# Kernel tuning notes

Hardware: AMD Instinct MI355X
Metric: run time of the kernel (lower is better)

## Reference

```python
import jax, jax.numpy as jnp
import numpy as np

DIM = 1024
HEADS = 16
DIM_HEAD = 64
INNER = HEADS * DIM_HEAD  # 1024
EPS = 1e-5


def layer_norm(x, g, b):
    mu = jnp.mean(x, axis=-1, keepdims=True)
    var = jnp.var(x, axis=-1, keepdims=True)
    return (x - mu) * jax.lax.rsqrt(var + EPS) * g + b


def setup_inputs() -> dict:
    key = jax.random.key(0)
    ks = jax.random.split(key, 8)
    s = 0.02
    return {
        "x": jax.random.normal(ks[0], (2, 2048, DIM), dtype=jnp.float32),
        "w_qkv": jax.random.normal(ks[1], (DIM, 3 * INNER), dtype=jnp.float32) * s,
        "w_out": jax.random.normal(ks[2], (INNER, DIM), dtype=jnp.float32) * s,
        "b_out": jnp.zeros((DIM,), jnp.float32),
        "g1": jnp.ones((DIM,), jnp.float32),
        "bt1": jnp.zeros((DIM,), jnp.float32),
        "g2": jnp.ones((DIM,), jnp.float32),
        "bt2": jnp.zeros((DIM,), jnp.float32),
        "w1": jax.random.normal(ks[3], (DIM, DIM), dtype=jnp.float32) * s,  # ff hidden = dim_out = DIM
        "b1": jnp.zeros((DIM,), jnp.float32),
        "w2": jax.random.normal(ks[4], (DIM, DIM), dtype=jnp.float32) * s,
        "b2": jnp.zeros((DIM,), jnp.float32),
    }


def reference(x, w_qkv, w_out, b_out, g1, bt1, g2, bt2, w1, b1, w2, b2):
    b, n, _ = x.shape
    scale = DIM_HEAD ** (-0.5)
    x_in = x
    xl = layer_norm(x, g1, bt1)
    qkv = xl @ w_qkv  # [b, n, 3*inner]
    q, k, v = jnp.split(qkv, 3, axis=-1)
    def split_heads(t):
        return t.reshape(b, n, HEADS, DIM_HEAD).transpose(0, 2, 1, 3)  # b h n d
    q, k, v = map(split_heads, (q, k, v))
    dots = jnp.einsum('bhid,bhjd->bhij', q, k) * scale
    attn = jax.nn.softmax(dots, axis=-1)
    out = jnp.einsum('bhij,bhjd->bhid', attn, v)
    out = out.transpose(0, 2, 1, 3).reshape(b, n, INNER)
    out = out @ w_out + b_out
    out = out + x_in
    h = layer_norm(out, g2, bt2)
    h = jax.nn.gelu(h @ w1 + b1, approximate=False) @ w2 + b2
    return h + out
```

## Files before the change

kernel.cpp:

```cpp
#include <hip/hip_runtime.h>
#include <math.h>

typedef __attribute__((ext_vector_type(4))) float f32x4;
typedef __attribute__((ext_vector_type(8))) short bf16x8;
typedef __attribute__((ext_vector_type(8))) unsigned short u16x8;

#define DIM 1024
#define SEQ 2048
#define NHEADS 16
#define DH 64

__device__ __forceinline__ unsigned short f2bf(float f) {
    unsigned int u = __builtin_bit_cast(unsigned int, f);
    u += 0x7fffu + ((u >> 16) & 1u);
    return (unsigned short)(u >> 16);
}

__device__ __forceinline__ float bf2f(unsigned short s) {
    unsigned int u = (unsigned int)s << 16;
    return __builtin_bit_cast(float, u);
}

__device__ __forceinline__ unsigned int cvt_pk_bf16(float lo, float hi) {
    unsigned int r;
    asm("v_cvt_pk_bf16_f32 %0, %1, %2" : "=v"(r) : "v"(lo), "v"(hi));
    return r;
}

__device__ __forceinline__ float fexp2(float x) {
    float r;
    asm("v_exp_f32 %0, %1" : "=v"(r) : "v"(x));
    return r;
}

__device__ __forceinline__ void gld16(const unsigned short* g, unsigned short* l) {
    __builtin_amdgcn_global_load_lds((const __attribute__((address_space(1))) void*)g,
                                     (__attribute__((address_space(3))) void*)l, 16, 0, 0);
}

__global__ __launch_bounds__(256) void wtrans_all(const float* __restrict__ wq,
                                                  const float* __restrict__ wo,
                                                  const float* __restrict__ wf1,
                                                  const float* __restrict__ wf2,
                                                  unsigned short* __restrict__ oq,
                                                  unsigned short* __restrict__ oo,
                                                  unsigned short* __restrict__ of1,
                                                  unsigned short* __restrict__ of2, float sc) {
    int z = blockIdx.z;
    int bxi = blockIdx.x;
    if (z > 0 && bxi >= 32) return;
    const float* w = z == 0 ? wq : z == 1 ? wo : z == 2 ? wf1 : wf2;
    unsigned short* wt = z == 0 ? oq : z == 1 ? oo : z == 2 ? of1 : of2;
    int N = z == 0 ? 3072 : 1024;
    int scale_n = z == 0 ? 1024 : 0;
    const int K = 1024;
    __shared__ float t[32][33];
    int tid = threadIdx.x;
    int n0 = bxi * 32, k0 = blockIdx.y * 32;
    int c = tid & 31, rb = tid >> 5;
#pragma unroll
    for (int i = 0; i < 4; ++i) {
        int r = rb + i * 8;
        t[r][c] = w[(size_t)(k0 + r) * N + n0 + c];
    }
    __syncthreads();
#pragma unroll
    for (int i = 0; i < 4; ++i) {
        int r = rb + i * 8;
        float v = t[c][r];
        if (n0 + r < scale_n) v *= sc;
        wt[(size_t)(n0 + r) * K + k0 + c] = f2bf(v);
    }
}

__global__ __launch_bounds__(256) void ln_kernel(const float* __restrict__ x,
                                                 const float* __restrict__ g,
                                                 const float* __restrict__ bt,
                                                 unsigned short* __restrict__ o) {
    int row = blockIdx.x, tid = threadIdx.x;
    const float4* xr = (const float4*)(x + (size_t)row * DIM);
    float4 v = xr[tid];
    float s1 = v.x + v.y + v.z + v.w;
    float s2 = v.x * v.x + v.y * v.y + v.z * v.z + v.w * v.w;
#pragma unroll
    for (int m = 32; m >= 1; m >>= 1) {
        s1 += __shfl_xor(s1, m);
        s2 += __shfl_xor(s2, m);
    }
    __shared__ float r1[4], r2[4];
    int w = tid >> 6;
    if ((tid & 63) == 0) { r1[w] = s1; r2[w] = s2; }
    __syncthreads();
    s1 = r1[0] + r1[1] + r1[2] + r1[3];
    s2 = r2[0] + r2[1] + r2[2] + r2[3];
    float mu = s1 * (1.0f / DIM);
    float var = s2 * (1.0f / DIM) - mu * mu;
    float rstd = rsqrtf(var + 1e-5f);
    float4 g4 = ((const float4*)g)[tid];
    float4 b4 = ((const float4*)bt)[tid];
    ushort4 ov;
    ov.x = f2bf((v.x - mu) * rstd * g4.x + b4.x);
    ov.y = f2bf((v.y - mu) * rstd * g4.y + b4.y);
    ov.z = f2bf((v.z - mu) * rstd * g4.z + b4.z);
    ov.w = f2bf((v.w - mu) * rstd * g4.w + b4.w);
    *(ushort4*)(o + (size_t)row * DIM + tid * 4) = ov;
}

template <int BN, int BK, int OBF, int BIAS, int GELU_, int RESID>
__global__ __launch_bounds__(256) void gemm_kernel(const unsigned short* __restrict__ A,
                                                   const unsigned short* __restrict__ BT,
                                                   void* __restrict__ C,
                                                   const float* __restrict__ bias,
                                                   const float* __restrict__ resid,
                                                   int M, int N, int K, int nbx) {
    constexpr int U = BK / 8;
    constexpr int NAU = 128 * U;
    constexpr int NBU = BN * U;
    constexpr int PT = (NAU + NBU) / 256;
    constexpr int NJ = BN / 32;
    constexpr int KK = BK / 32;
    __shared__ unsigned short As[3][128 * BK];
    __shared__ unsigned short Bs[3][BN * BK];
    int tid = threadIdx.x;
    int lane = tid & 63, w = tid >> 6;
    int l15 = lane & 15, lhi = lane >> 4;
    int nwg = gridDim.x, wg = blockIdx.x;
    int swz = (wg & 7) * (nwg >> 3) + (wg >> 3);
    int bx = swz % nbx, by = swz / nbx;
    int row0 = by * 128, col0 = bx * BN;
    int wrow = (w >> 1) * 64, wcol = (w & 1) * (16 * NJ);
    f32x4 zero = {0.f, 0.f, 0.f, 0.f};
    f32x4 acc[4][NJ];
#pragma unroll
    for (int i = 0; i < 4; ++i)
#pragma unroll
        for (int j = 0; j < NJ; ++j) acc[i][j] = zero;
    auto stage = [&](int buf, int kt) {
#pragma unroll
        for (int p = 0; p < PT; ++p) {
            if (p * 256 < NAU) {
                int u = tid + p * 256;
                int r = u / U, cu = u % U;
                int scu = cu ^ (r & (U - 1));
                gld16(A + (size_t)(row0 + r) * K + kt * BK + scu * 8, &As[buf][0] + u * 8);
            } else {
                int ub = tid + p * 256 - NAU;
                int r = ub / U, cu = ub % U;
                int scu = cu ^ (r & (U - 1));
                gld16(BT + (size_t)(col0 + r) * K + kt * BK + scu * 8, &Bs[buf][0] + ub * 8);
            }
        }
    };
    int nk = K / BK;
    stage(0, 0);
    stage(1, 1);
    asm volatile("s_waitcnt vmcnt(%0)" ::"i"(PT) : "memory");
    __builtin_amdgcn_s_barrier();
    __builtin_amdgcn_sched_barrier(0);
    int cur = 0;
    for (int kt = 0; kt < nk; ++kt) {
        int nxt2 = cur + 2 >= 3 ? cur - 1 : cur + 2;
        if (kt + 2 < nk) stage(nxt2, kt + 2);
        const unsigned short* Ab = &As[cur][0];
        const unsigned short* Bb = &Bs[cur][0];
        bf16x8 af[4][KK], bfr[NJ][KK];
#pragma unroll
        for (int i = 0; i < 4; ++i)
#pragma unroll
            for (int kk = 0; kk < KK; ++kk) {
                int rr = wrow + i * 16 + l15;
                int up = (kk * 4 + lhi) ^ (rr & (U - 1));
                af[i][kk] = *(const bf16x8*)&Ab[rr * BK + up * 8];
            }
#pragma unroll
        for (int j = 0; j < NJ; ++j)
#pragma unroll
            for (int kk = 0; kk < KK; ++kk) {
                int rr = wcol + j * 16 + l15;
                int up = (kk * 4 + lhi) ^ (rr & (U - 1));
                bfr[j][kk] = *(const bf16x8*)&Bb[rr * BK + up * 8];
            }
#pragma unroll
        for (int kk = 0; kk < KK; ++kk)
#pragma unroll
            for (int i = 0; i < 4; ++i)
#pragma unroll
                for (int j = 0; j < NJ; ++j)
                    acc[i][j] = __builtin_amdgcn_mfma_f32_16x16x32_bf16(af[i][kk], bfr[j][kk],
                                                                        acc[i][j], 0, 0, 0);
        __builtin_amdgcn_sched_barrier(0);
        if (kt + 1 < nk) {
            if (kt + 2 < nk)
                asm volatile("s_waitcnt vmcnt(%0)" ::"i"(PT) : "memory");
            else
                asm volatile("s_waitcnt vmcnt(0)" ::: "memory");
            __builtin_amdgcn_s_barrier();
            __builtin_amdgcn_sched_barrier(0);
        }
        cur = cur + 1 == 3 ? 0 : cur + 1;
    }
#pragma unroll
    for (int i = 0; i < 4; ++i)
#pragma unroll
        for (int j = 0; j < NJ; ++j)
#pragma unroll
            for (int r = 0; r < 4; ++r) {
                int row = row0 + wrow + i * 16 + lhi * 4 + r;
                int col = col0 + wcol + j * 16 + l15;
                float v = acc[i][j][r];
                if (BIAS) v += bias[col];
                if (GELU_) v = 0.5f * v * (1.0f + erff(v * 0.70710678118f));
                if (RESID) v += resid[(size_t)row * N + col];
                if (OBF)
                    ((unsigned short*)C)[(size_t)row * N + col] = f2bf(v);
                else
                    ((float*)C)[(size_t)row * N + col] = v;
            }
}

__global__ __launch_bounds__(256) void vtrans_kernel(const unsigned short* __restrict__ qkv,
                                                     unsigned short* __restrict__ vt) {
    __shared__ unsigned short t[64 * 72];
    int tid = threadIdx.x;
    int nt = blockIdx.x & 31, h = (blockIdx.x >> 5) & 15, b = blockIdx.x >> 9;
#pragma unroll
    for (int p = 0; p < 2; ++p) {
        int c = tid + p * 256;
        int n = c >> 3, s = (c & 7) * 8;
        *(uint4*)&t[n * 72 + s] =
            *(const uint4*)(qkv + (size_t)(b * SEQ + nt * 64 + n) * 3072 + 2048 + h * 64 + s);
    }
    __syncthreads();
#pragma unroll
    for (int p = 0; p < 2; ++p) {
        int c = tid + p * 256;
        int d = c >> 3, s0 = (c & 7) * 8;
        u16x8 val;
#pragma unroll
        for (int j = 0; j < 8; ++j) {
            int s = s0 + j;
            int sig = (s & 32) | ((s & 4) << 2) | ((s & 24) >> 1) | (s & 3);
            val[j] = t[sig * 72 + d];
        }
        *(u16x8*)(vt + ((size_t)(b * NHEADS + h) * DH + d) * SEQ + nt * 64 + s0) = val;
    }
}

__global__ __launch_bounds__(256) void attn_kernel(const unsigned short* __restrict__ qkv,
                                                   const unsigned short* __restrict__ vt,
                                                   unsigned short* __restrict__ po,
                                                   float* __restrict__ pl) {
    __shared__ unsigned short Ks[64 * 64];
    __shared__ unsigned short Vs[64 * 64];
    int tid = threadIdx.x;
    int lane = tid & 63, w = tid >> 6;
    int l15 = lane & 15, lhi = lane >> 4;
    int wg = blockIdx.x;
    int swz = (wg & 7) * 128 + (wg >> 3);
    int qt = swz & 15, half = (swz >> 4) & 1, h = (swz >> 5) & 15, b = swz >> 9;
    bf16x8 qf[2][2];
#pragma unroll
    for (int qg = 0; qg < 2; ++qg) {
        const unsigned short* qb =
            qkv + (size_t)(b * SEQ + qt * 128 + w * 32 + qg * 16 + l15) * 3072 + h * DH;
        qf[qg][0] = *(const bf16x8*)(qb + lhi * 8);
        qf[qg][1] = *(const bf16x8*)(qb + 32 + lhi * 8);
    }
    f32x4 zero = {0.f, 0.f, 0.f, 0.f};
    f32x4 oacc[2][4], lacc[2];
#pragma unroll
    for (int qg = 0; qg < 2; ++qg) {
        lacc[qg] = zero;
#pragma unroll
        for (int i = 0; i < 4; ++i) oacc[qg][i] = zero;
    }
    const short one_s = (short)0x3F80;
    bf16x8 ones = {one_s, one_s, one_s, one_s, one_s, one_s, one_s, one_s};
    int srow = tid >> 3;
    int scx = (tid & 7) ^ (srow & 7);
    const unsigned short* kb = qkv + (size_t)b * SEQ * 3072 + 1024 + h * DH;
    const unsigned short* vb = vt + (size_t)(b * NHEADS + h) * DH * SEQ;
    const unsigned short* k0 = kb + (size_t)srow * 3072 + scx * 8;
    const unsigned short* v0 = vb + (size_t)srow * SEQ + scx * 8;
    auto stage = [&](int kg) {
        unsigned short* lk = &Ks[0] + tid * 8;
        unsigned short* lv = &Vs[0] + tid * 8;
        gld16(k0 + (size_t)kg * 64 * 3072, lk);
        gld16(k0 + ((size_t)kg * 64 + 32) * 3072, lk + 2048);
        gld16(v0 + kg * 64, lv);
        gld16(v0 + (size_t)32 * SEQ + kg * 64, lv + 2048);
    };
    int kx = l15 & 7;
    const int NT2 = SEQ / 64 / 2;
    for (int kt = 0; kt < NT2; ++kt) {
        stage(half * NT2 + kt);
        asm volatile("s_waitcnt vmcnt(0)" ::: "memory");
        __builtin_amdgcn_s_barrier();
        __builtin_amdgcn_sched_barrier(0);
        f32x4 sacc[2][4];
#pragma unroll
        for (int nt = 0; nt < 4; ++nt) {
            bf16x8 kf0 = *(const bf16x8*)&Ks[(nt * 16 + l15) * 64 + ((lhi ^ kx) * 8)];
            bf16x8 kf1 = *(const bf16x8*)&Ks[(nt * 16 + l15) * 64 + (((4 + lhi) ^ kx) * 8)];
#pragma unroll
            for (int qg = 0; qg < 2; ++qg) {
                f32x4 z = __builtin_amdgcn_mfma_f32_16x16x32_bf16(kf0, qf[qg][0], zero, 0, 0, 0);
                sacc[qg][nt] = __builtin_amdgcn_mfma_f32_16x16x32_bf16(kf1, qf[qg][1], z, 0, 0, 0);
            }
        }
        bf16x8 pf[2][2];
#pragma unroll
        for (int qg = 0; qg < 2; ++qg)
#pragma unroll
            for (int kc = 0; kc < 2; ++kc) {
                union { bf16x8 v; unsigned int u[4]; } pu;
                pu.u[0] = cvt_pk_bf16(fexp2(sacc[qg][2 * kc][0]), fexp2(sacc[qg][2 * kc][1]));
                pu.u[1] = cvt_pk_bf16(fexp2(sacc[qg][2 * kc][2]), fexp2(sacc[qg][2 * kc][3]));
                pu.u[2] = cvt_pk_bf16(fexp2(sacc[qg][2 * kc + 1][0]), fexp2(sacc[qg][2 * kc + 1][1]));
                pu.u[3] = cvt_pk_bf16(fexp2(sacc[qg][2 * kc + 1][2]), fexp2(sacc[qg][2 * kc + 1][3]));
                pf[qg][kc] = pu.v;
            }
#pragma unroll
        for (int dt = 0; dt < 4; ++dt)
#pragma unroll
            for (int kc = 0; kc < 2; ++kc) {
                bf16x8 vf = *(const bf16x8*)&Vs[(dt * 16 + l15) * 64 + (((kc * 4 + lhi) ^ kx) * 8)];
#pragma unroll
                for (int qg = 0; qg < 2; ++qg)
                    oacc[qg][dt] =
                        __builtin_amdgcn_mfma_f32_16x16x32_bf16(vf, pf[qg][kc], oacc[qg][dt], 0, 0, 0);
            }
#pragma unroll
        for (int qg = 0; qg < 2; ++qg) {
            lacc[qg] = __builtin_amdgcn_mfma_f32_16x16x32_bf16(ones, pf[qg][0], lacc[qg], 0, 0, 0);
            lacc[qg] = __builtin_amdgcn_mfma_f32_16x16x32_bf16(ones, pf[qg][1], lacc[qg], 0, 0, 0);
        }
        __builtin_amdgcn_sched_barrier(0);
        if (kt + 1 < NT2) {
            __builtin_amdgcn_s_barrier();
            __builtin_amdgcn_sched_barrier(0);
        }
    }
#pragma unroll
    for (int qg = 0; qg < 2; ++qg) {
        int rrow = b * SEQ + qt * 128 + w * 32 + qg * 16 + l15;
        unsigned short* pob = po + ((size_t)half * 4096 + rrow) * DIM + h * DH;
#pragma unroll
        for (int dt = 0; dt < 4; ++dt) {
            ushort4 st;
            st.x = f2bf(oacc[qg][dt][0]);
            st.y = f2bf(oacc[qg][dt][1]);
            st.z = f2bf(oacc[qg][dt][2]);
            st.w = f2bf(oacc[qg][dt][3]);
            *(ushort4*)(pob + dt * 16 + lhi * 4) = st;
        }
        if (lhi == 0) pl[((size_t)half * 4096 + rrow) * NHEADS + h] = lacc[qg][0];
    }
}

__global__ __launch_bounds__(256) void attn_combine(const unsigned short* __restrict__ po,
                                                    const float* __restrict__ pl,
                                                    unsigned short* __restrict__ o) {
    int r = blockIdx.x, tid = threadIdx.x;
    int d0 = tid * 4, h = d0 >> 6;
    ushort4 a = *(const ushort4*)(po + (size_t)r * DIM + d0);
    ushort4 c = *(const ushort4*)(po + (size_t)(4096 + r) * DIM + d0);
    float rl = 1.0f / (pl[(size_t)r * NHEADS + h] + pl[(size_t)(4096 + r) * NHEADS + h]);
    ushort4 ov;
    ov.x = f2bf((bf2f(a.x) + bf2f(c.x)) * rl);
    ov.y = f2bf((bf2f(a.y) + bf2f(c.y)) * rl);
    ov.z = f2bf((bf2f(a.z) + bf2f(c.z)) * rl);
    ov.w = f2bf((bf2f(a.w) + bf2f(c.w)) * rl);
    *(ushort4*)(o + (size_t)r * DIM + d0) = ov;
}

extern "C" void kernel_launch(void* const* d_in, const int* in_sizes, int n_in,
                              void* d_out, int out_size, void* d_ws, size_t ws_size,
                              hipStream_t stream) {
    (void)in_sizes; (void)n_in; (void)out_size; (void)ws_size;
    const float* x = (const float*)d_in[0];
    const float* w_qkv = (const float*)d_in[1];
    const float* w_out = (const float*)d_in[2];
    const float* b_out = (const float*)d_in[3];
    const float* g1 = (const float*)d_in[4];
    const float* bt1 = (const float*)d_in[5];
    const float* g2 = (const float*)d_in[6];
    const float* bt2 = (const float*)d_in[7];
    const float* w1 = (const float*)d_in[8];
    const float* b1 = (const float*)d_in[9];
    const float* w2 = (const float*)d_in[10];
    const float* b2 = (const float*)d_in[11];
    float* out = (float*)d_out;

    char* ws = (char*)d_ws;
    size_t off = 0;
    auto alloc = [&](size_t bytes) {
        void* p = ws + off;
        off += (bytes + 255) & ~(size_t)255;
        return p;
    };
    const int R = 2 * SEQ;
    unsigned short* xl    = (unsigned short*)alloc((size_t)R * DIM * 2);
    unsigned short* wqkvT = (unsigned short*)alloc((size_t)3 * DIM * DIM * 2);
    unsigned short* woutT = (unsigned short*)alloc((size_t)DIM * DIM * 2);
    unsigned short* w1T   = (unsigned short*)alloc((size_t)DIM * DIM * 2);
    unsigned short* w2T   = (unsigned short*)alloc((size_t)DIM * DIM * 2);
    unsigned short* qkvb  = (unsigned short*)alloc((size_t)R * 3 * DIM * 2);
    unsigned short* vtb   = (unsigned short*)alloc((size_t)R * DIM * 2);
    unsigned short* attO  = (unsigned short*)alloc((size_t)R * DIM * 2);
    unsigned short* h2    = (unsigned short*)alloc((size_t)R * DIM * 2);
    unsigned short* ffn1  = (unsigned short*)alloc((size_t)R * DIM * 2);
    unsigned short* po = (unsigned short*)alloc((size_t)2 * R * DIM * 2);
    float* pl = (float*)alloc((size_t)2 * R * NHEADS * 4);

    const float CS = 0.125f * 1.44269504f;
    wtrans_all<<<dim3(96, 32, 4), 256, 0, stream>>>(w_qkv, w_out, w1, w2, wqkvT, woutT, w1T, w2T, CS);

    ln_kernel<<<R, 256, 0, stream>>>(x, g1, bt1, xl);
    gemm_kernel<128, 32, 1, 0, 0, 0><<<dim3((3 * DIM / 128) * (R / 128)), 256, 0, stream>>>(
        xl, wqkvT, qkvb, nullptr, nullptr, R, 3 * DIM, DIM, 3 * DIM / 128);
    vtrans_kernel<<<2 * NHEADS * (SEQ / 64), 256, 0, stream>>>(qkvb, vtb);
    attn_kernel<<<2 * NHEADS * (SEQ / 128) * 2, 256, 0, stream>>>(qkvb, vtb, po, pl);
    attn_combine<<<R, 256, 0, stream>>>(po, pl, attO);
    gemm_kernel<64, 64, 0, 1, 0, 1><<<dim3((DIM / 64) * (R / 128)), 256, 0, stream>>>(
        attO, woutT, out, b_out, x, R, DIM, DIM, DIM / 64);
    ln_kernel<<<R, 256, 0, stream>>>(out, g2, bt2, h2);
    gemm_kernel<64, 64, 1, 1, 1, 0><<<dim3((DIM / 64) * (R / 128)), 256, 0, stream>>>(
        h2, w1T, ffn1, b1, nullptr, R, DIM, DIM, DIM / 64);
    gemm_kernel<64, 64, 0, 1, 0, 1><<<dim3((DIM / 64) * (R / 128)), 256, 0, stream>>>(
        ffn1, w2T, out, b2, out, R, DIM, DIM, DIM / 64);
}
```

Before: 173.1 us.

## Fuse first LayerNorm into weight-transpose kernel and V-transpose into QKV GEMM epilogue

```diff
diff --git a/kernel.cpp b/kernel.cpp
--- a/kernel.cpp
+++ b/kernel.cpp
@@ -38,24 +38,58 @@
                                      (__attribute__((address_space(3))) void*)l, 16, 0, 0);
 }
 
-__global__ __launch_bounds__(256) void wtrans_all(const float* __restrict__ wq,
-                                                  const float* __restrict__ wo,
-                                                  const float* __restrict__ wf1,
-                                                  const float* __restrict__ wf2,
-                                                  unsigned short* __restrict__ oq,
-                                                  unsigned short* __restrict__ oo,
-                                                  unsigned short* __restrict__ of1,
-                                                  unsigned short* __restrict__ of2, float sc) {
+__global__ __launch_bounds__(256) void wtrans_ln(const float* __restrict__ wq,
+                                                 const float* __restrict__ wo,
+                                                 const float* __restrict__ wf1,
+                                                 const float* __restrict__ wf2,
+                                                 unsigned short* __restrict__ oq,
+                                                 unsigned short* __restrict__ oo,
+                                                 unsigned short* __restrict__ of1,
+                                                 unsigned short* __restrict__ of2, float sc,
+                                                 const float* __restrict__ x,
+                                                 const float* __restrict__ g1,
+                                                 const float* __restrict__ bt1,
+                                                 unsigned short* __restrict__ xl) {
     int z = blockIdx.z;
     int bxi = blockIdx.x;
-    if (z > 0 && bxi >= 32) return;
+    int tid = threadIdx.x;
+    if (z == 4) {
+        int row = blockIdx.y * 128 + bxi;
+        const float4* xr = (const float4*)(x + (size_t)row * DIM);
+        float4 v = xr[tid];
+        float s1 = v.x + v.y + v.z + v.w;
+        float s2 = v.x * v.x + v.y * v.y + v.z * v.z + v.w * v.w;
+#pragma unroll
+        for (int m = 32; m >= 1; m >>= 1) {
+            s1 += __shfl_xor(s1, m);
+            s2 += __shfl_xor(s2, m);
+        }
+        __shared__ float r1[4], r2[4];
+        int w = tid >> 6;
+        if ((tid & 63) == 0) { r1[w] = s1; r2[w] = s2; }
+        __syncthreads();
+        s1 = r1[0] + r1[1] + r1[2] + r1[3];
+        s2 = r2[0] + r2[1] + r2[2] + r2[3];
+        float mu = s1 * (1.0f / DIM);
+        float var = s2 * (1.0f / DIM) - mu * mu;
+        float rstd = rsqrtf(var + 1e-5f);
+        float4 g4 = ((const float4*)g1)[tid];
+        float4 b4 = ((const float4*)bt1)[tid];
+        ushort4 ov;
+        ov.x = f2bf((v.x - mu) * rstd * g4.x + b4.x);
+        ov.y = f2bf((v.y - mu) * rstd * g4.y + b4.y);
+        ov.z = f2bf((v.z - mu) * rstd * g4.z + b4.z);
+        ov.w = f2bf((v.w - mu) * rstd * g4.w + b4.w);
+        *(ushort4*)(xl + (size_t)row * DIM + tid * 4) = ov;
+        return;
+    }
+    if (bxi >= (z == 0 ? 96 : 32)) return;
     const float* w = z == 0 ? wq : z == 1 ? wo : z == 2 ? wf1 : wf2;
     unsigned short* wt = z == 0 ? oq : z == 1 ? oo : z == 2 ? of1 : of2;
     int N = z == 0 ? 3072 : 1024;
     int scale_n = z == 0 ? 1024 : 0;
     const int K = 1024;
     __shared__ float t[32][33];
-    int tid = threadIdx.x;
     int n0 = bxi * 32, k0 = blockIdx.y * 32;
     int c = tid & 31, rb = tid >> 5;
 #pragma unroll
@@ -106,12 +140,13 @@
     *(ushort4*)(o + (size_t)row * DIM + tid * 4) = ov;
 }
 
-template <int BN, int BK, int OBF, int BIAS, int GELU_, int RESID>
+template <int BN, int BK, int OBF, int BIAS, int GELU_, int RESID, int VT>
 __global__ __launch_bounds__(256) void gemm_kernel(const unsigned short* __restrict__ A,
                                                    const unsigned short* __restrict__ BT,
                                                    void* __restrict__ C,
                                                    const float* __restrict__ bias,
                                                    const float* __restrict__ resid,
+                                                   unsigned short* __restrict__ vt,
                                                    int M, int N, int K, int nbx) {
     constexpr int U = BK / 8;
     constexpr int NAU = 128 * U;
@@ -119,8 +154,9 @@
     constexpr int PT = (NAU + NBU) / 256;
     constexpr int NJ = BN / 32;
     constexpr int KK = BK / 32;
-    __shared__ unsigned short As[3][128 * BK];
-    __shared__ unsigned short Bs[3][BN * BK];
+    extern __shared__ char smem[];
+    unsigned short* As = (unsigned short*)smem;
+    unsigned short* Bs = As + 3 * 128 * BK;
     int tid = threadIdx.x;
     int lane = tid & 63, w = tid >> 6;
     int l15 = lane & 15, lhi = lane >> 4;
@@ -142,12 +178,12 @@
                 int u = tid + p * 256;
                 int r = u / U, cu = u % U;
                 int scu = cu ^ (r & (U - 1));
-                gld16(A + (size_t)(row0 + r) * K + kt * BK + scu * 8, &As[buf][0] + u * 8);
+                gld16(A + (size_t)(row0 + r) * K + kt * BK + scu * 8, As + buf * 128 * BK + u * 8);
             } else {
                 int ub = tid + p * 256 - NAU;
                 int r = ub / U, cu = ub % U;
                 int scu = cu ^ (r & (U - 1));
-                gld16(BT + (size_t)(col0 + r) * K + kt * BK + scu * 8, &Bs[buf][0] + ub * 8);
+                gld16(BT + (size_t)(col0 + r) * K + kt * BK + scu * 8, Bs + buf * BN * BK + ub * 8);
             }
         }
     };
@@ -161,8 +197,8 @@
     for (int kt = 0; kt < nk; ++kt) {
         int nxt2 = cur + 2 >= 3 ? cur - 1 : cur + 2;
         if (kt + 2 < nk) stage(nxt2, kt + 2);
-        const unsigned short* Ab = &As[cur][0];
-        const unsigned short* Bb = &Bs[cur][0];
+        const unsigned short* Ab = As + cur * 128 * BK;
+        const unsigned short* Bb = Bs + cur * BN * BK;
         bf16x8 af[4][KK], bfr[NJ][KK];
 #pragma unroll
         for (int i = 0; i < 4; ++i)
@@ -199,6 +235,29 @@
         }
         cur = cur + 1 == 3 ? 0 : cur + 1;
     }
+    if (VT && col0 >= 2048) {
+        __syncthreads();
+        unsigned short* Ct = (unsigned short*)smem;
+#pragma unroll
+        for (int i = 0; i < 4; ++i)
+#pragma unroll
+            for (int j = 0; j < NJ; ++j)
+#pragma unroll
+                for (int r = 0; r < 4; ++r)
+                    Ct[(wrow + i * 16 + lhi * 4 + r) * 130 + (wcol + j * 16 + l15)] =
+                        f2bf(acc[i][j][r]);
+        __syncthreads();
+        int l = tid & 63, wv = tid >> 6;
+        int sig = (l & 32) | ((l & 4) << 2) | ((l & 24) >> 1) | (l & 3);
+        int b = row0 >> 11, n0 = row0 & 2047;
+        int h0 = (col0 - 2048) >> 6;
+        for (int c = wv * 64; c < wv * 64 + 64; ++c) {
+            int ntl = c & 1, hl = (c >> 1) & 1, d = c >> 2;
+            unsigned short v = Ct[(ntl * 64 + sig) * 130 + hl * 64 + d];
+            vt[((size_t)(b * NHEADS + h0 + hl) * DH + d) * SEQ + n0 + ntl * 64 + l] = v;
+        }
+        return;
+    }
 #pragma unroll
     for (int i = 0; i < 4; ++i)
 #pragma unroll
@@ -216,34 +275,6 @@
                 else
                     ((float*)C)[(size_t)row * N + col] = v;
             }
-}
-
-__global__ __launch_bounds__(256) void vtrans_kernel(const unsigned short* __restrict__ qkv,
-                                                     unsigned short* __restrict__ vt) {
-    __shared__ unsigned short t[64 * 72];
-    int tid = threadIdx.x;
-    int nt = blockIdx.x & 31, h = (blockIdx.x >> 5) & 15, b = blockIdx.x >> 9;
-#pragma unroll
-    for (int p = 0; p < 2; ++p) {
-        int c = tid + p * 256;
-        int n = c >> 3, s = (c & 7) * 8;
-        *(uint4*)&t[n * 72 + s] =
-            *(const uint4*)(qkv + (size_t)(b * SEQ + nt * 64 + n) * 3072 + 2048 + h * 64 + s);
-    }
-    __syncthreads();
-#pragma unroll
-    for (int p = 0; p < 2; ++p) {
-        int c = tid + p * 256;
-        int d = c >> 3, s0 = (c & 7) * 8;
-        u16x8 val;
-#pragma unroll
-        for (int j = 0; j < 8; ++j) {
-            int s = s0 + j;
-            int sig = (s & 32) | ((s & 4) << 2) | ((s & 24) >> 1) | (s & 3);
-            val[j] = t[sig * 72 + d];
-        }
-        *(u16x8*)(vt + ((size_t)(b * NHEADS + h) * DH + d) * SEQ + nt * 64 + s0) = val;
-    }
 }
 
 __global__ __launch_bounds__(256) void attn_kernel(const unsigned short* __restrict__ qkv,
@@ -414,19 +445,21 @@
     float* pl = (float*)alloc((size_t)2 * R * NHEADS * 4);
 
     const float CS = 0.125f * 1.44269504f;
-    wtrans_all<<<dim3(96, 32, 4), 256, 0, stream>>>(w_qkv, w_out, w1, w2, wqkvT, woutT, w1T, w2T, CS);
-
-    ln_kernel<<<R, 256, 0, stream>>>(x, g1, bt1, xl);
-    gemm_kernel<128, 32, 1, 0, 0, 0><<<dim3((3 * DIM / 128) * (R / 128)), 256, 0, stream>>>(
-        xl, wqkvT, qkvb, nullptr, nullptr, R, 3 * DIM, DIM, 3 * DIM / 128);
-    vtrans_kernel<<<2 * NHEADS * (SEQ / 64), 256, 0, stream>>>(qkvb, vtb);
+    wtrans_ln<<<dim3(128, 32, 5), 256, 0, stream>>>(w_qkv, w_out, w1, w2, wqkvT, woutT, w1T, w2T,
+                                                    CS, x, g1, bt1, xl);
+
+    const unsigned int SH_QKV = (3 * 128 * 32 + 3 * 128 * 32) * 2;
+    const unsigned int SH_FFN = (3 * 128 * 64 + 3 * 64 * 64) * 2;
+    gemm_kernel<128, 32, 1, 0, 0, 0, 1>
+        <<<dim3((3 * DIM / 128) * (R / 128)), 256, SH_QKV, stream>>>(
+            xl, wqkvT, qkvb, nullptr, nullptr, vtb, R, 3 * DIM, DIM, 3 * DIM / 128);
     attn_kernel<<<2 * NHEADS * (SEQ / 128) * 2, 256, 0, stream>>>(qkvb, vtb, po, pl);
     attn_combine<<<R, 256, 0, stream>>>(po, pl, attO);
-    gemm_kernel<64, 64, 0, 1, 0, 1><<<dim3((DIM / 64) * (R / 128)), 256, 0, stream>>>(
-        attO, woutT, out, b_out, x, R, DIM, DIM, DIM / 64);
+    gemm_kernel<64, 64, 0, 1, 0, 1, 0><<<dim3((DIM / 64) * (R / 128)), 256, SH_FFN, stream>>>(
+        attO, woutT, out, b_out, x, nullptr, R, DIM, DIM, DIM / 64);
     ln_kernel<<<R, 256, 0, stream>>>(out, g2, bt2, h2);
-    gemm_kernel<64, 64, 1, 1, 1, 0><<<dim3((DIM / 64) * (R / 128)), 256, 0, stream>>>(
-        h2, w1T, ffn1, b1, nullptr, R, DIM, DIM, DIM / 64);
-    gemm_kernel<64, 64, 0, 1, 0, 1><<<dim3((DIM / 64) * (R / 128)), 256, 0, stream>>>(
-        ffn1, w2T, out, b2, out, R, DIM, DIM, DIM / 64);
-}
+    gemm_kernel<64, 64, 1, 1, 1, 0, 0><<<dim3((DIM / 64) * (R / 128)), 256, SH_FFN, stream>>>(
+        h2, w1T, ffn1, b1, nullptr, nullptr, R, DIM, DIM, DIM / 64);
+    gemm_kernel<64, 64, 0, 1, 0, 1, 0><<<dim3((DIM / 64) * (R / 128)), 256, SH_FFN, stream>>>(
+        ffn1, w2T, out, b2, out, nullptr, R, DIM, DIM, DIM / 64);
+}
```

Result: faster. 168.3 us (-2.8%).
